# Kernel optimization log

Measured on AMD Instinct MI355X. Metric: run time of the kernel, lower is better.

Reference implementation:

```python
import jax, jax.numpy as jnp
import numpy as np

ROUNDS = 64   # sequential hash rounds
HIDDEN = 256  # state width (bits) and square matrix size
B = 65536     # batch of independent inputs being hashed in parallel


def setup_inputs() -> dict:
    key = jax.random.key(0)
    k1, k2, k3 = jax.random.split(key, 3)
    # state bits in {0,1}, shape [B, HIDDEN]
    state = jax.random.randint(k1, (B, HIDDEN), 0, 2).astype(jnp.float32)
    # ternary matrices in {-1,0,1} (bytes % 3 - 1 in the original), [ROUNDS, HIDDEN, HIDDEN]
    matrices = (jax.random.randint(k2, (ROUNDS, HIDDEN, HIDDEN), 0, 3) - 1).astype(jnp.float32)
    # per-round noise bits in {0,1}, [ROUNDS, HIDDEN]
    noise = jax.random.randint(k3, (ROUNDS, HIDDEN), 0, 2).astype(jnp.float32)
    return {"state": state, "matrices": matrices, "noise": noise}


def reference(state, matrices, noise):
    # Each round: state = floor(state @ W_r^T + noise_r) mod 2
    def step(s, wn):
        W, n = wn  # W: [HIDDEN, HIDDEN], n: [HIDDEN]
        s = jnp.remainder(jnp.floor(jnp.matmul(s, W.T) + n), 2.0)
        return s, None

    out, _ = jax.lax.scan(step, state, (matrices, noise))
    return out  # [B, HIDDEN] final bit state
```

## Files before the change

kernel.cpp:

```cpp
#include <hip/hip_runtime.h>
#include <stdint.h>

#define ROUNDS 64
#define HIDDEN 256
#define BATCH  65536

typedef int   v4i  __attribute__((ext_vector_type(4)));
typedef int   v8i  __attribute__((ext_vector_type(8)));
typedef float v16f __attribute__((ext_vector_type(16)));
typedef unsigned long long u64;


#define WB_OFF   0u
#define NB_OFF   524288u
#define G1M_OFF  526336u
#define G1V_OFF  657408u
#define G2M_OFF  657920u
#define G2V_OFF  690688u
#define FM_OFF   690816u
#define FV_OFF   699008u
#define WPK_OFF  699072u
#define NF_OFF   731840u

__host__ __device__ constexpr int rho(int n) {
  return 4 * (n >> 4) + (n & 3) + 8 * ((n >> 2) & 3);
}

__host__ __device__ constexpr float bias_q(int q) {
  return (q == 0) ? 6291456.0f
       : (q == 1) ? 393216.0f
       : (q == 2) ? 24576.0f
                  : 1536.0f;
}

__global__ __launch_bounds__(256) void bitpack(const float* __restrict__ mat,
                                               const float* __restrict__ noi,
                                               u64* __restrict__ wb,
                                               u64* __restrict__ nb) {
  unsigned blk = blockIdx.x;
  if (blk >= 16384u) {
    unsigned tg = (blk - 16384u) * 256u + threadIdx.x;
    u64 m = __ballot(noi[tg] != 0.f);
    if ((threadIdx.x & 63u) == 0u) nb[tg >> 6] = m;
    return;
  }
  unsigned tg = blk * 256u + threadIdx.x;
  u64 m = __ballot(mat[tg] != 0.f);
  if ((threadIdx.x & 63u) == 0u) wb[tg >> 6] = m;
}

__global__ __launch_bounds__(1024) void fold(const u64* __restrict__ inM,
                                             const u64* __restrict__ inV,
                                             u64* __restrict__ outM,
                                             u64* __restrict__ outV,
                                             int chain) {
  __shared__ u64 A[256][5];
  __shared__ u64 tbl[64][16][5];
  __shared__ u64 avec[4];
  const int tid = threadIdx.x;
  const int w = tid >> 8;
  const int i = tid & 255;
  const int base = blockIdx.x * chain;

  A[i][w] = inM[(size_t)base * 1024 + i * 4 + w];
  if (tid < 4) avec[tid] = inV[base * 4 + tid];
  __syncthreads();

  for (int j = 1; j < chain; ++j) {
    const u64* Bm = inM + (size_t)(base + j) * 1024;
    u64 br[4];
#pragma unroll
    for (int q = 0; q < 4; ++q) br[q] = Bm[i * 4 + q];
    u64 bword = (tid < 256) ? inV[(size_t)(base + j) * 4 + (i >> 6)] : 0ull;
    u64 av0 = avec[0], av1 = avec[1], av2 = avec[2], av3 = avec[3];

    {
      const int c = tid >> 4, m = tid & 15;
      u64 t0 = 0, t1 = 0, t2 = 0, t3 = 0;
#pragma unroll
      for (int jj = 0; jj < 4; ++jj)
        if (m & (1 << jj)) {
          t0 ^= A[4 * c + jj][0]; t1 ^= A[4 * c + jj][1];
          t2 ^= A[4 * c + jj][2]; t3 ^= A[4 * c + jj][3];
        }
      tbl[c][m][0] = t0; tbl[c][m][1] = t1; tbl[c][m][2] = t2; tbl[c][m][3] = t3;
    }
    __syncthreads();

    u64 a0 = 0, a1 = 0, a2 = 0, a3 = 0;
#pragma unroll
    for (int c = 0; c < 64; c += 4) {
      unsigned n0 = (unsigned)(br[(c + 0) >> 4] >> (((c + 0) & 15) * 4)) & 15u;
      unsigned n1 = (unsigned)(br[(c + 1) >> 4] >> (((c + 1) & 15) * 4)) & 15u;
      unsigned n2 = (unsigned)(br[(c + 2) >> 4] >> (((c + 2) & 15) * 4)) & 15u;
      unsigned n3 = (unsigned)(br[(c + 3) >> 4] >> (((c + 3) & 15) * 4)) & 15u;
      a0 ^= tbl[c + 0][n0][w];
      a1 ^= tbl[c + 1][n1][w];
      a2 ^= tbl[c + 2][n2][w];
      a3 ^= tbl[c + 3][n3][w];
    }
    u64 acc = (a0 ^ a1) ^ (a2 ^ a3);

    u64 mask = 0;
    if (tid < 256) {
      int p = __popcll(br[0] & av0) + __popcll(br[1] & av1) +
              __popcll(br[2] & av2) + __popcll(br[3] & av3);
      int bit = ((int)((bword >> (i & 63)) & 1ull)) ^ (p & 1);
      mask = __ballot(bit);
    }
    __syncthreads();
    A[i][w] = acc;
    if (tid < 256 && (i & 63) == 0) avec[i >> 6] = mask;
    __syncthreads();
  }

  outM[(size_t)blockIdx.x * 1024 + i * 4 + w] = A[i][w];
  if (tid < 4) outV[blockIdx.x * 4 + tid] = avec[tid];
}

__global__ __launch_bounds__(256) void packm(const u64* __restrict__ FM,
                                             const u64* __restrict__ FV,
                                             uint32_t* __restrict__ wpk,
                                             float* __restrict__ nf) {
  if (blockIdx.x == 8) {
    unsigned tid = threadIdx.x;
    unsigned j = tid & 15u, lh = (tid >> 4) & 1u, mt = tid >> 5;
    unsigned row = mt * 32u + (j & 3u) + 8u * (j >> 2) + 4u * lh;
    nf[tid] = (float)((FV[row >> 6] >> (row & 63u)) & 1ull);
    return;
  }
  unsigned tg = blockIdx.x * 256u + threadIdx.x;
  unsigned kwin = tg & 7u, row = tg >> 3;
  const u64* Mr = FM + row * 4;
  uint32_t w[4] = {0, 0, 0, 0};
#pragma unroll
  for (int n = 0; n < 32; ++n) {
    int k = (int)kwin * 32 + rho(n);
    uint32_t bit = (uint32_t)((Mr[k >> 6] >> (k & 63)) & 1ull);
    w[n >> 3] |= (bit * 2u) << ((n & 7) * 4);
  }
  unsigned mt = row >> 5, lh = kwin & 1u, ks = kwin >> 1;
  unsigned lane = lh * 32u + (row & 31u);
  *(uint4*)(wpk + (((mt * 4u + ks) * 64u + lane) << 2)) =
      make_uint4(w[0], w[1], w[2], w[3]);
}

__global__ __launch_bounds__(512, 4) void hash1(const uint32_t* __restrict__ wpk,
                                                const float* __restrict__ nf,
                                                const float* __restrict__ sta,
                                                float* __restrict__ out) {
  __shared__ uint8_t T[2][8][128][16];
  const int t = threadIdx.x;
  const int wv = __builtin_amdgcn_readfirstlane(t >> 6);
  const int lane = t & 63;
  const int l31 = lane & 31;
  const int lh = lane >> 5;
  const int el0 = blockIdx.x * 128;

#pragma unroll
  for (int i = 0; i < 16; ++i) {
    unsigned flat = (unsigned)i * 512u + t;
    unsigned el = flat >> 6, k4 = flat & 63u;
    float4 f = ((const float4*)(sta + (size_t)el0 * 256))[flat];
    uint32_t v = ((f.x != 0.f) ? 0x2u : 0u) | ((f.y != 0.f) ? 0x20u : 0u) |
                 ((f.z != 0.f) ? 0x200u : 0u) | ((f.w != 0.f) ? 0x2000u : 0u);
    unsigned KB = k4 >> 3, k4c = k4 & 7u;
    unsigned byteoff = (k4c & 1u) * 8u + 2u * (k4c >> 1);
    *(uint16_t*)&T[0][KB][el][byteoff] = (uint16_t)v;
  }
  __syncthreads();

  v4i ap[4];
  {
    const uint32_t* wb = wpk + ((wv * 4) << 8);
#pragma unroll
    for (int ks = 0; ks < 4; ++ks) ap[ks] = *(const v4i*)(wb + ks * 256 + lane * 4);
  }
  v16f NZ = *(const v16f*)(nf + (wv * 2 + lh) * 16);

  v16f acc[4];
  __builtin_amdgcn_s_setprio(1);
#pragma unroll
  for (int ks = 0; ks < 4; ++ks) {
    v8i A8 = __builtin_shufflevector(ap[ks], ap[ks], 0, 1, 2, 3, -1, -1, -1, -1);
    const int kb = 2 * ks + lh;
#pragma unroll
    for (int tn = 0; tn < 4; ++tn) {
      v4i b4 = *(const v4i*)&T[0][kb][tn * 32 + l31][0];
      v8i B8 = __builtin_shufflevector(b4, b4, 0, 1, 2, 3, -1, -1, -1, -1);
      acc[tn] = __builtin_amdgcn_mfma_scale_f32_32x32x64_f8f6f4(
          A8, B8, (ks == 0) ? NZ : acc[tn], 4, 4, 0, 127, 0, 127);
    }
  }
  __builtin_amdgcn_s_setprio(0);

#pragma unroll
  for (int tn = 0; tn < 4; ++tn) {
#define PB(j)                                                          \
  (__builtin_bit_cast(uint32_t, acc[tn][j] + bias_q((j) & 3)) &        \
   (2u << (4 * ((j) & 3))))
    uint32_t u0 = PB(0) | PB(1) | PB(2) | PB(3);
    uint32_t u1 = PB(4) | PB(5) | PB(6) | PB(7);
    uint32_t u2 = PB(8) | PB(9) | PB(10) | PB(11);
    uint32_t u3 = PB(12) | PB(13) | PB(14) | PB(15);
#undef PB
    *(uint2*)&T[1][wv][tn * 32 + l31][lh * 8] =
        make_uint2(u0 | (u1 << 16), u2 | (u3 << 16));
  }
  __syncthreads();

#pragma unroll
  for (int i = 0; i < 16; ++i) {
    unsigned flat = (unsigned)i * 512u + t;
    unsigned el = flat >> 6, k4 = flat & 63u;
    unsigned KB = k4 >> 3, k4c = k4 & 7u;
    unsigned byteoff = (k4c & 1u) * 8u + 2u * (k4c >> 1);
    uint32_t v = *(const uint16_t*)&T[1][KB][el][byteoff];
    float4 o = make_float4((float)((v >> 1) & 1u), (float)((v >> 5) & 1u),
                           (float)((v >> 9) & 1u), (float)((v >> 13) & 1u));
    ((float4*)(out + (size_t)el0 * 256))[flat] = o;
  }
}

extern "C" void kernel_launch(void* const* d_in, const int* in_sizes, int n_in,
                              void* d_out, int out_size, void* d_ws, size_t ws_size,
                              hipStream_t stream) {
  const float* sta = (const float*)d_in[0];
  const float* mat = (const float*)d_in[1];
  const float* noi = (const float*)d_in[2];
  uint8_t* wsb = (uint8_t*)d_ws;

  u64* Wb       = (u64*)(wsb + WB_OFF);
  u64* nb       = (u64*)(wsb + NB_OFF);
  u64* G1M      = (u64*)(wsb + G1M_OFF);
  u64* G1V      = (u64*)(wsb + G1V_OFF);
  u64* G2M      = (u64*)(wsb + G2M_OFF);
  u64* G2V      = (u64*)(wsb + G2V_OFF);
  u64* FM       = (u64*)(wsb + FM_OFF);
  u64* FV       = (u64*)(wsb + FV_OFF);
  uint32_t* wpk = (uint32_t*)(wsb + WPK_OFF);
  float* nf     = (float*)(wsb + NF_OFF);

  bitpack<<<16448, 256, 0, stream>>>(mat, noi, Wb, nb);
  fold<<<16, 1024, 0, stream>>>(Wb, nb, G1M, G1V, 4);
  fold<<<4, 1024, 0, stream>>>(G1M, G1V, G2M, G2V, 4);
  fold<<<1, 1024, 0, stream>>>(G2M, G2V, FM, FV, 4);
  packm<<<9, 256, 0, stream>>>(FM, FV, wpk, nf);
  hash1<<<512, 512, 0, stream>>>(wpk, nf, sta, (float*)d_out);
}
```

Before: 225.7 us.

## Fuse fold levels and packing into one cooperative kernel with grid sync

Replaces the three fold launches and the packm launch with a single cooperative kernel. It runs the 4-way fold tree with grid.sync between levels and does the final packing from shared memory. The B-operand matrices for the whole chain are also prefetched into registers before the loop. This removes three kernel launch gaps and a global round trip for the final matrix, at the cost of the cooperative launch overhead and grid barriers.

```diff
diff --git a/kernel.cpp b/kernel.cpp
--- a/kernel.cpp
+++ b/kernel.cpp
@@ -1,4 +1,5 @@
 #include <hip/hip_runtime.h>
+#include <hip/hip_cooperative_groups.h>
 #include <stdint.h>
 
 #define ROUNDS 64
@@ -9,6 +10,8 @@
 typedef int   v8i  __attribute__((ext_vector_type(8)));
 typedef float v16f __attribute__((ext_vector_type(16)));
 typedef unsigned long long u64;
+
+namespace cg = cooperative_groups;
 
 
 #define WB_OFF   0u
@@ -17,10 +20,8 @@
 #define G1V_OFF  657408u
 #define G2M_OFF  657920u
 #define G2V_OFF  690688u
-#define FM_OFF   690816u
-#define FV_OFF   699008u
-#define WPK_OFF  699072u
-#define NF_OFF   731840u
+#define WPK_OFF  690816u
+#define NF_OFF   723584u
 
 __host__ __device__ constexpr int rho(int n) {
   return 4 * (n >> 4) + (n & 3) + 8 * ((n >> 2) & 3);
@@ -49,100 +50,121 @@
   if ((threadIdx.x & 63u) == 0u) wb[tg >> 6] = m;
 }
 
-__global__ __launch_bounds__(1024) void fold(const u64* __restrict__ inM,
-                                             const u64* __restrict__ inV,
-                                             u64* __restrict__ outM,
-                                             u64* __restrict__ outV,
-                                             int chain) {
+__device__ __forceinline__ void fold_chain(u64 (&A)[256][5], u64 (&tbl)[64][16][5],
+                                           u64 (&avec)[4],
+                                           const u64* __restrict__ inM,
+                                           const u64* __restrict__ inV,
+                                           int base, int tid, int w, int i) {
+  A[i][w] = inM[(size_t)base * 1024 + i * 4 + w];
+  if (tid < 4) avec[tid] = inV[base * 4 + tid];
+  u64 br[3][4], bw[3];
+#pragma unroll
+  for (int j = 0; j < 3; ++j) {
+    const u64* Bm = inM + (size_t)(base + 1 + j) * 1024;
+#pragma unroll
+    for (int q = 0; q < 4; ++q) br[j][q] = Bm[i * 4 + q];
+    bw[j] = (tid < 256) ? inV[(size_t)(base + 1 + j) * 4 + (i >> 6)] : 0ull;
+  }
+  __syncthreads();
+
+#pragma unroll
+  for (int j = 0; j < 3; ++j) {
+    u64 av0 = avec[0], av1 = avec[1], av2 = avec[2], av3 = avec[3];
+    {
+      const int c = tid >> 4, m = tid & 15;
+      u64 t0 = 0, t1 = 0, t2 = 0, t3 = 0;
+#pragma unroll
+      for (int jj = 0; jj < 4; ++jj)
+        if (m & (1 << jj)) {
+          t0 ^= A[4 * c + jj][0]; t1 ^= A[4 * c + jj][1];
+          t2 ^= A[4 * c + jj][2]; t3 ^= A[4 * c + jj][3];
+        }
+      tbl[c][m][0] = t0; tbl[c][m][1] = t1; tbl[c][m][2] = t2; tbl[c][m][3] = t3;
+    }
+    __syncthreads();
+
+    u64 a0 = 0, a1 = 0, a2 = 0, a3 = 0;
+#pragma unroll
+    for (int c = 0; c < 64; c += 4) {
+      unsigned n0 = (unsigned)(br[j][(c + 0) >> 4] >> (((c + 0) & 15) * 4)) & 15u;
+      unsigned n1 = (unsigned)(br[j][(c + 1) >> 4] >> (((c + 1) & 15) * 4)) & 15u;
+      unsigned n2 = (unsigned)(br[j][(c + 2) >> 4] >> (((c + 2) & 15) * 4)) & 15u;
+      unsigned n3 = (unsigned)(br[j][(c + 3) >> 4] >> (((c + 3) & 15) * 4)) & 15u;
+      a0 ^= tbl[c + 0][n0][w];
+      a1 ^= tbl[c + 1][n1][w];
+      a2 ^= tbl[c + 2][n2][w];
+      a3 ^= tbl[c + 3][n3][w];
+    }
+    u64 acc = (a0 ^ a1) ^ (a2 ^ a3);
+
+    u64 mask = 0;
+    if (tid < 256) {
+      int p = __popcll(br[j][0] & av0) + __popcll(br[j][1] & av1) +
+              __popcll(br[j][2] & av2) + __popcll(br[j][3] & av3);
+      int bit = ((int)((bw[j] >> (i & 63)) & 1ull)) ^ (p & 1);
+      mask = __ballot(bit);
+    }
+    __syncthreads();
+    A[i][w] = acc;
+    if (tid < 256 && (i & 63) == 0) avec[i >> 6] = mask;
+    __syncthreads();
+  }
+}
+
+__global__ __launch_bounds__(1024) void foldall(const u64* __restrict__ Wb,
+                                                const u64* __restrict__ nb,
+                                                u64* __restrict__ G1M,
+                                                u64* __restrict__ G1V,
+                                                u64* __restrict__ G2M,
+                                                u64* __restrict__ G2V,
+                                                uint32_t* __restrict__ wpk,
+                                                float* __restrict__ nf) {
   __shared__ u64 A[256][5];
   __shared__ u64 tbl[64][16][5];
   __shared__ u64 avec[4];
   const int tid = threadIdx.x;
   const int w = tid >> 8;
   const int i = tid & 255;
-  const int base = blockIdx.x * chain;
-
-  A[i][w] = inM[(size_t)base * 1024 + i * 4 + w];
-  if (tid < 4) avec[tid] = inV[base * 4 + tid];
-  __syncthreads();
-
-  for (int j = 1; j < chain; ++j) {
-    const u64* Bm = inM + (size_t)(base + j) * 1024;
-    u64 br[4];
-#pragma unroll
-    for (int q = 0; q < 4; ++q) br[q] = Bm[i * 4 + q];
-    u64 bword = (tid < 256) ? inV[(size_t)(base + j) * 4 + (i >> 6)] : 0ull;
-    u64 av0 = avec[0], av1 = avec[1], av2 = avec[2], av3 = avec[3];
-
-    {
-      const int c = tid >> 4, m = tid & 15;
-      u64 t0 = 0, t1 = 0, t2 = 0, t3 = 0;
-#pragma unroll
-      for (int jj = 0; jj < 4; ++jj)
-        if (m & (1 << jj)) {
-          t0 ^= A[4 * c + jj][0]; t1 ^= A[4 * c + jj][1];
-          t2 ^= A[4 * c + jj][2]; t3 ^= A[4 * c + jj][3];
-        }
-      tbl[c][m][0] = t0; tbl[c][m][1] = t1; tbl[c][m][2] = t2; tbl[c][m][3] = t3;
-    }
-    __syncthreads();
-
-    u64 a0 = 0, a1 = 0, a2 = 0, a3 = 0;
-#pragma unroll
-    for (int c = 0; c < 64; c += 4) {
-      unsigned n0 = (unsigned)(br[(c + 0) >> 4] >> (((c + 0) & 15) * 4)) & 15u;
-      unsigned n1 = (unsigned)(br[(c + 1) >> 4] >> (((c + 1) & 15) * 4)) & 15u;
-      unsigned n2 = (unsigned)(br[(c + 2) >> 4] >> (((c + 2) & 15) * 4)) & 15u;
-      unsigned n3 = (unsigned)(br[(c + 3) >> 4] >> (((c + 3) & 15) * 4)) & 15u;
-      a0 ^= tbl[c + 0][n0][w];
-      a1 ^= tbl[c + 1][n1][w];
-      a2 ^= tbl[c + 2][n2][w];
-      a3 ^= tbl[c + 3][n3][w];
-    }
-    u64 acc = (a0 ^ a1) ^ (a2 ^ a3);
-
-    u64 mask = 0;
+  cg::grid_group grid = cg::this_grid();
+
+  fold_chain(A, tbl, avec, Wb, nb, blockIdx.x * 4, tid, w, i);
+  G1M[(size_t)blockIdx.x * 1024 + i * 4 + w] = A[i][w];
+  if (tid < 4) G1V[blockIdx.x * 4 + tid] = avec[tid];
+  __threadfence();
+  grid.sync();
+
+  if (blockIdx.x < 4) {
+    fold_chain(A, tbl, avec, G1M, G1V, blockIdx.x * 4, tid, w, i);
+    G2M[(size_t)blockIdx.x * 1024 + i * 4 + w] = A[i][w];
+    if (tid < 4) G2V[blockIdx.x * 4 + tid] = avec[tid];
+  }
+  __threadfence();
+  grid.sync();
+
+  if (blockIdx.x == 0) {
+    fold_chain(A, tbl, avec, G2M, G2V, 0, tid, w, i);
+#pragma unroll
+    for (int it = 0; it < 2; ++it) {
+      unsigned tg = (unsigned)it * 1024u + tid;
+      unsigned kwin = tg & 7u, row = tg >> 3;
+      uint32_t wd[4] = {0, 0, 0, 0};
+#pragma unroll
+      for (int n = 0; n < 32; ++n) {
+        int k = (int)kwin * 32 + rho(n);
+        uint32_t bit = (uint32_t)((A[row][k >> 6] >> (k & 63)) & 1ull);
+        wd[n >> 3] |= (bit * 2u) << ((n & 7) * 4);
+      }
+      unsigned mt = row >> 5, lhh = kwin & 1u, ks = kwin >> 1;
+      unsigned lane = lhh * 32u + (row & 31u);
+      *(uint4*)(wpk + (((mt * 4u + ks) * 64u + lane) << 2)) =
+          make_uint4(wd[0], wd[1], wd[2], wd[3]);
+    }
     if (tid < 256) {
-      int p = __popcll(br[0] & av0) + __popcll(br[1] & av1) +
-              __popcll(br[2] & av2) + __popcll(br[3] & av3);
-      int bit = ((int)((bword >> (i & 63)) & 1ull)) ^ (p & 1);
-      mask = __ballot(bit);
-    }
-    __syncthreads();
-    A[i][w] = acc;
-    if (tid < 256 && (i & 63) == 0) avec[i >> 6] = mask;
-    __syncthreads();
-  }
-
-  outM[(size_t)blockIdx.x * 1024 + i * 4 + w] = A[i][w];
-  if (tid < 4) outV[blockIdx.x * 4 + tid] = avec[tid];
-}
-
-__global__ __launch_bounds__(256) void packm(const u64* __restrict__ FM,
-                                             const u64* __restrict__ FV,
-                                             uint32_t* __restrict__ wpk,
-                                             float* __restrict__ nf) {
-  if (blockIdx.x == 8) {
-    unsigned tid = threadIdx.x;
-    unsigned j = tid & 15u, lh = (tid >> 4) & 1u, mt = tid >> 5;
-    unsigned row = mt * 32u + (j & 3u) + 8u * (j >> 2) + 4u * lh;
-    nf[tid] = (float)((FV[row >> 6] >> (row & 63u)) & 1ull);
-    return;
-  }
-  unsigned tg = blockIdx.x * 256u + threadIdx.x;
-  unsigned kwin = tg & 7u, row = tg >> 3;
-  const u64* Mr = FM + row * 4;
-  uint32_t w[4] = {0, 0, 0, 0};
-#pragma unroll
-  for (int n = 0; n < 32; ++n) {
-    int k = (int)kwin * 32 + rho(n);
-    uint32_t bit = (uint32_t)((Mr[k >> 6] >> (k & 63)) & 1ull);
-    w[n >> 3] |= (bit * 2u) << ((n & 7) * 4);
-  }
-  unsigned mt = row >> 5, lh = kwin & 1u, ks = kwin >> 1;
-  unsigned lane = lh * 32u + (row & 31u);
-  *(uint4*)(wpk + (((mt * 4u + ks) * 64u + lane) << 2)) =
-      make_uint4(w[0], w[1], w[2], w[3]);
+      unsigned j = tid & 15u, lhh = (tid >> 4) & 1u, mt = (unsigned)tid >> 5;
+      unsigned row = mt * 32u + (j & 3u) + 8u * (j >> 2) + 4u * lhh;
+      nf[tid] = (float)((avec[row >> 6] >> (row & 63u)) & 1ull);
+    }
+  }
 }
 
 __global__ __launch_bounds__(512, 4) void hash1(const uint32_t* __restrict__ wpk,
@@ -236,15 +258,14 @@
   u64* G1V      = (u64*)(wsb + G1V_OFF);
   u64* G2M      = (u64*)(wsb + G2M_OFF);
   u64* G2V      = (u64*)(wsb + G2V_OFF);
-  u64* FM       = (u64*)(wsb + FM_OFF);
-  u64* FV       = (u64*)(wsb + FV_OFF);
   uint32_t* wpk = (uint32_t*)(wsb + WPK_OFF);
   float* nf     = (float*)(wsb + NF_OFF);
 
   bitpack<<<16448, 256, 0, stream>>>(mat, noi, Wb, nb);
-  fold<<<16, 1024, 0, stream>>>(Wb, nb, G1M, G1V, 4);
-  fold<<<4, 1024, 0, stream>>>(G1M, G1V, G2M, G2V, 4);
-  fold<<<1, 1024, 0, stream>>>(G2M, G2V, FM, FV, 4);
-  packm<<<9, 256, 0, stream>>>(FM, FV, wpk, nf);
+
+  void* kargs[8] = {&Wb, &nb, &G1M, &G1V, &G2M, &G2V, &wpk, &nf};
+  hipLaunchCooperativeKernel((const void*)foldall, dim3(16), dim3(1024), kargs,
+                             0, stream);
+
   hash1<<<512, 512, 0, stream>>>(wpk, nf, sta, (float*)d_out);
 }
```

New measurement: 270.0 us. +19.7%, slower.
